# Kernel optimization log

Measured on AMD Instinct MI355X. Metric: run time of the kernel, lower is better.

## Reference

```python
import jax, jax.numpy as jnp
import numpy as np

E, H, L = 1280, 20, 8192
D = E // H


def setup_inputs() -> dict:
    key = jax.random.key(0)
    ks = jax.random.split(key, 12)
    inp = {
        "hidden_states": jax.random.normal(ks[0], (1, 1, E), jnp.float32),
        "position_ids": jax.random.randint(ks[1], (1,), 0, L, jnp.int64),
        "k_cache": jax.random.normal(ks[2], (1, H, L, D), jnp.float32),
        "v_cache": jax.random.normal(ks[3], (1, H, L, D), jnp.float32),
        "Wq": jax.random.normal(ks[4], (E, E), jnp.float32) * 0.02,
        "bq": jax.random.normal(ks[5], (E,), jnp.float32) * 0.02,
        "Wk": jax.random.normal(ks[6], (E, E), jnp.float32) * 0.02,
        "Wv": jax.random.normal(ks[7], (E, E), jnp.float32) * 0.02,
        "bv": jax.random.normal(ks[8], (E,), jnp.float32) * 0.02,
        "Wo": jax.random.normal(ks[9], (E, E), jnp.float32) * 0.02,
        "bo": jax.random.normal(ks[10], (E,), jnp.float32) * 0.02,
    }
    return inp


def reference(hidden_states, position_ids, k_cache, v_cache, Wq, bq, Wk, Wv, bv, Wo, bo):
    # hidden_states: [1,1,E]; k_cache/v_cache: [1,H,L,D]; position_ids: [1] int
    h = k_cache.shape[1]
    d = k_cache.shape[3]
    l = k_cache.shape[2]
    e = h * d
    scale = jnp.asarray(d, hidden_states.dtype) ** -0.5

    def split_heads(x):  # [1,1,E] -> [1,H,1,D]
        return x.reshape(1, 1, h, d).transpose(0, 2, 1, 3)

    q = split_heads((hidden_states @ Wq.T + bq) * scale)
    k_new = split_heads(hidden_states @ Wk.T)          # k_proj has no bias
    v_new = split_heads(hidden_states @ Wv.T + bv)

    pos = position_ids.reshape(())
    positions = jnp.arange(l)
    write_mask = (positions == pos)[None, None, :, None]   # [1,1,L,1]
    # masked broadcast-update of the KV cache (same math as cache*(1-m)+new*m)
    new_k_cache = jnp.where(write_mask, k_new, k_cache)    # [1,H,L,D]
    new_v_cache = jnp.where(write_mask, v_new, v_cache)

    scores = jnp.einsum('bhqd,bhkd->bhqk', q, new_k_cache)  # [1,H,1,L]
    causal = jnp.where(positions[None, None, None, :] <= pos,
                       jnp.asarray(0.0, scores.dtype),
                       jnp.asarray(-1e9, scores.dtype))
    attn = jax.nn.softmax(scores + causal, axis=-1)
    out = jnp.einsum('bhqk,bhkd->bhqd', attn, new_v_cache)  # [1,H,1,D]
    out = out.transpose(0, 2, 1, 3).reshape(1, 1, e)
    out = out @ Wo.T + bo
    return out, new_k_cache, new_v_cache
```

## Files before the change

kernel.cpp:

```cpp
#include <hip/hip_runtime.h>

#define E 1280
#define H 20
#define L 8192
#define D 64
#define CHUNK 256
#define NCHUNK (L / CHUNK)

__global__ void qkv_kernel(const float* __restrict__ hs,
                           const float* __restrict__ Wq, const float* __restrict__ bq,
                           const float* __restrict__ Wk,
                           const float* __restrict__ Wv, const float* __restrict__ bv,
                           float* __restrict__ qkv) {
    int row_global = blockIdx.x * 4 + (threadIdx.x >> 6);
    int lane = threadIdx.x & 63;
    int mat = row_global / E;
    int row = row_global - mat * E;
    const float* W = (mat == 0) ? Wq : (mat == 1) ? Wk : Wv;
    const float4* Wrow = (const float4*)(W + (size_t)row * E);
    const float4* h4 = (const float4*)hs;
    float sum = 0.f;
#pragma unroll
    for (int i = 0; i < 5; ++i) {
        int idx = lane + 64 * i;
        float4 w4 = Wrow[idx];
        float4 x4 = h4[idx];
        sum += w4.x * x4.x + w4.y * x4.y + w4.z * x4.z + w4.w * x4.w;
    }
#pragma unroll
    for (int off = 32; off > 0; off >>= 1) sum += __shfl_down(sum, off, 64);
    if (lane == 0) {
        float val;
        if (mat == 0)      val = (sum + bq[row]) * 0.125f;
        else if (mat == 1) val = sum;
        else               val = sum + bv[row];
        qkv[mat * E + row] = val;
    }
}

__global__ void kv_kernel(const float* __restrict__ kc, const float* __restrict__ vc,
                          const float* __restrict__ qkv, const int* __restrict__ pos_p,
                          float* __restrict__ out_k, float* __restrict__ out_v,
                          float* __restrict__ cmax, float* __restrict__ csum,
                          float* __restrict__ o_part) {
    int h = blockIdx.x / NCHUNK;
    int c = blockIdx.x - h * NCHUNK;
    int pos = pos_p[0];
    int wave = threadIdx.x >> 6;
    int lane = threadIdx.x & 63;
    int rr = lane >> 4;
    int cc = lane & 15;

    __shared__ float s_lds[CHUNK];
    __shared__ float sacc[4][D];
    __shared__ float smax[4];
    __shared__ float spsum[4];

    float4 q4  = ((const float4*)qkv)[h * 16 + cc];
    float4 kn4 = ((const float4*)(qkv + E))[h * 16 + cc];
    float4 vn4 = ((const float4*)(qkv + 2 * E))[h * 16 + cc];

    size_t base = ((size_t)h * L + (size_t)c * CHUNK) * D;
    const float* kbase = kc + base;
    const float* vbase = vc + base;
    float* okbase = out_k + base;
    float* ovbase = out_v + base;
    int l0 = c * CHUNK;

    float lmax = -INFINITY;
#pragma unroll 4
    for (int it = 0; it < CHUNK / 16; ++it) {
        int r = it * 16 + wave * 4 + rr;
        int l = l0 + r;
        float4 k4 = ((const float4*)(kbase + r * D))[cc];
        if (l == pos) k4 = kn4;
        ((float4*)(okbase + r * D))[cc] = k4;
        float p = q4.x * k4.x + q4.y * k4.y + q4.z * k4.z + q4.w * k4.w;
        p += __shfl_xor(p, 1, 16);
        p += __shfl_xor(p, 2, 16);
        p += __shfl_xor(p, 4, 16);
        p += __shfl_xor(p, 8, 16);
        float s = (l <= pos) ? p : -INFINITY;
        if (cc == 0) s_lds[r] = s;
        lmax = fmaxf(lmax, s);
    }
#pragma unroll
    for (int off = 32; off > 0; off >>= 1)
        lmax = fmaxf(lmax, __shfl_xor(lmax, off, 64));
    if (lane == 0) smax[wave] = lmax;
    __syncthreads();
    float m = fmaxf(fmaxf(smax[0], smax[1]), fmaxf(smax[2], smax[3]));

    float4 acc = {0.f, 0.f, 0.f, 0.f};
    float psum = 0.f;
#pragma unroll 4
    for (int it = 0; it < CHUNK / 16; ++it) {
        int r = it * 16 + wave * 4 + rr;
        int l = l0 + r;
        float4 v4 = ((const float4*)(vbase + r * D))[cc];
        if (l == pos) v4 = vn4;
        ((float4*)(ovbase + r * D))[cc] = v4;
        float p = (l <= pos) ? __expf(s_lds[r] - m) : 0.f;
        acc.x += p * v4.x; acc.y += p * v4.y; acc.z += p * v4.z; acc.w += p * v4.w;
        if (cc == 0) psum += p;
    }
    acc.x += __shfl_xor(acc.x, 16, 64); acc.y += __shfl_xor(acc.y, 16, 64);
    acc.z += __shfl_xor(acc.z, 16, 64); acc.w += __shfl_xor(acc.w, 16, 64);
    acc.x += __shfl_xor(acc.x, 32, 64); acc.y += __shfl_xor(acc.y, 32, 64);
    acc.z += __shfl_xor(acc.z, 32, 64); acc.w += __shfl_xor(acc.w, 32, 64);
    psum += __shfl_xor(psum, 16, 64);
    psum += __shfl_xor(psum, 32, 64);
    if (rr == 0) {
        ((float4*)&sacc[wave][cc * 4])[0] = acc;
        if (cc == 0) spsum[wave] = psum;
    }
    __syncthreads();
    if (threadIdx.x < D) {
        int d = threadIdx.x;
        float o = sacc[0][d] + sacc[1][d] + sacc[2][d] + sacc[3][d];
        o_part[((size_t)h * NCHUNK + c) * D + d] = o;
        if (d == 0) {
            cmax[h * NCHUNK + c] = m;
            csum[h * NCHUNK + c] = spsum[0] + spsum[1] + spsum[2] + spsum[3];
        }
    }
}

__global__ void combine_kernel(const float* __restrict__ cmax, const float* __restrict__ csum,
                               const float* __restrict__ o_part, float* __restrict__ attn_out) {
    int h = blockIdx.x;
    int d = threadIdx.x;
    float m = -INFINITY;
#pragma unroll
    for (int c = 0; c < NCHUNK; ++c) m = fmaxf(m, cmax[h * NCHUNK + c]);
    float denom = 0.f, o = 0.f;
#pragma unroll 4
    for (int c = 0; c < NCHUNK; ++c) {
        float mc = cmax[h * NCHUNK + c];
        float sc = (mc > -1e30f) ? __expf(mc - m) : 0.f;
        denom += csum[h * NCHUNK + c] * sc;
        o += o_part[((size_t)h * NCHUNK + c) * D + d] * sc;
    }
    attn_out[h * D + d] = o / denom;
}

__global__ void ogemv_kernel(const float* __restrict__ attn_out, const float* __restrict__ Wo,
                             const float* __restrict__ bo, float* __restrict__ out) {
    int row = blockIdx.x * 4 + (threadIdx.x >> 6);
    int lane = threadIdx.x & 63;
    const float4* Wrow = (const float4*)(Wo + (size_t)row * E);
    const float4* x4 = (const float4*)attn_out;
    float sum = 0.f;
#pragma unroll
    for (int i = 0; i < 5; ++i) {
        int idx = lane + 64 * i;
        float4 w4 = Wrow[idx];
        float4 a4 = x4[idx];
        sum += w4.x * a4.x + w4.y * a4.y + w4.z * a4.z + w4.w * a4.w;
    }
#pragma unroll
    for (int off = 32; off > 0; off >>= 1) sum += __shfl_down(sum, off, 64);
    if (lane == 0) out[row] = sum + bo[row];
}

extern "C" void kernel_launch(void* const* d_in, const int* in_sizes, int n_in,
                              void* d_out, int out_size, void* d_ws, size_t ws_size,
                              hipStream_t stream) {
    const float* hs  = (const float*)d_in[0];
    const int*   pos = (const int*)d_in[1];
    const float* kc  = (const float*)d_in[2];
    const float* vc  = (const float*)d_in[3];
    const float* Wq  = (const float*)d_in[4];
    const float* bq  = (const float*)d_in[5];
    const float* Wk  = (const float*)d_in[6];
    const float* Wv  = (const float*)d_in[7];
    const float* bv  = (const float*)d_in[8];
    const float* Wo  = (const float*)d_in[9];
    const float* bo  = (const float*)d_in[10];

    float* out   = (float*)d_out;
    float* out_k = out + E;
    float* out_v = out_k + (size_t)H * L * D;

    float* ws       = (float*)d_ws;
    float* qkv      = ws;
    float* cmax     = qkv + 3 * E;
    float* csum     = cmax + H * NCHUNK;
    float* o_part   = csum + H * NCHUNK;
    float* attn_out = o_part + (size_t)H * NCHUNK * D;

    qkv_kernel<<<3 * E / 4, 256, 0, stream>>>(hs, Wq, bq, Wk, Wv, bv, qkv);
    kv_kernel<<<H * NCHUNK, 256, 0, stream>>>(kc, vc, qkv, pos, out_k, out_v,
                                              cmax, csum, o_part);
    combine_kernel<<<H, 64, 0, stream>>>(cmax, csum, o_part, attn_out);
    ogemv_kernel<<<E / 4, 256, 0, stream>>>(attn_out, Wo, bo, out);
}
```

Measured before the change: 42.94 us.

## Halve attention chunk, use nontemporal cache-copy stores, and compute softmax weights through LDS

Chunk size drops from 256 to 128, doubling the number of blocks for the bandwidth-bound KV copy and attention pass. The per-row shuffle reductions of q·k are replaced by writing partial dot products to a padded LDS array, then one thread per row sums them and computes the exp weight once. The copies of the K and V caches into the outputs now use nontemporal stores so the streaming writes do not pollute cache. In exchange the kernel adds barriers and LDS traffic, and the combine step has twice as many partial results to merge.

```diff
diff --git a/kernel.cpp b/kernel.cpp
--- a/kernel.cpp
+++ b/kernel.cpp
@@ -4,8 +4,10 @@
 #define H 20
 #define L 8192
 #define D 64
-#define CHUNK 256
+#define CHUNK 128
 #define NCHUNK (L / CHUNK)
+
+typedef float f4 __attribute__((ext_vector_type(4)));
 
 __global__ void qkv_kernel(const float* __restrict__ hs,
                            const float* __restrict__ Wq, const float* __restrict__ bq,
@@ -46,15 +48,17 @@
     int h = blockIdx.x / NCHUNK;
     int c = blockIdx.x - h * NCHUNK;
     int pos = pos_p[0];
-    int wave = threadIdx.x >> 6;
-    int lane = threadIdx.x & 63;
-    int rr = lane >> 4;
-    int cc = lane & 15;
-
-    __shared__ float s_lds[CHUNK];
+    int tid = threadIdx.x;
+    int wave = tid >> 6;
+    int lane = tid & 63;
+    int cc = tid & 15;
+    int rg = tid >> 4;
+
+    __shared__ float s_part[CHUNK][17];
+    __shared__ float s_w[CHUNK];
+    __shared__ float smax4[4];
+    __shared__ float spsum[4];
     __shared__ float sacc[4][D];
-    __shared__ float smax[4];
-    __shared__ float spsum[4];
 
     float4 q4  = ((const float4*)qkv)[h * 16 + cc];
     float4 kn4 = ((const float4*)(qkv + E))[h * 16 + cc];
@@ -67,59 +71,66 @@
     float* ovbase = out_v + base;
     int l0 = c * CHUNK;
 
-    float lmax = -INFINITY;
-#pragma unroll 4
+#pragma unroll
     for (int it = 0; it < CHUNK / 16; ++it) {
-        int r = it * 16 + wave * 4 + rr;
+        int r = it * 16 + rg;
         int l = l0 + r;
         float4 k4 = ((const float4*)(kbase + r * D))[cc];
         if (l == pos) k4 = kn4;
-        ((float4*)(okbase + r * D))[cc] = k4;
-        float p = q4.x * k4.x + q4.y * k4.y + q4.z * k4.z + q4.w * k4.w;
-        p += __shfl_xor(p, 1, 16);
-        p += __shfl_xor(p, 2, 16);
-        p += __shfl_xor(p, 4, 16);
-        p += __shfl_xor(p, 8, 16);
-        float s = (l <= pos) ? p : -INFINITY;
-        if (cc == 0) s_lds[r] = s;
-        lmax = fmaxf(lmax, s);
-    }
+        f4 kv = {k4.x, k4.y, k4.z, k4.w};
+        __builtin_nontemporal_store(kv, (f4*)(okbase + r * D) + cc);
+        s_part[r][cc] = k4.x * q4.x + k4.y * q4.y + k4.z * q4.z + k4.w * q4.w;
+    }
+    __syncthreads();
+
+    float s = -INFINITY;
+    if (tid < CHUNK) {
+        float sum = 0.f;
+#pragma unroll
+        for (int i = 0; i < 16; ++i) sum += s_part[tid][i];
+        s = (l0 + tid <= pos) ? sum : -INFINITY;
+    }
+    float lm = s;
 #pragma unroll
     for (int off = 32; off > 0; off >>= 1)
-        lmax = fmaxf(lmax, __shfl_xor(lmax, off, 64));
-    if (lane == 0) smax[wave] = lmax;
-    __syncthreads();
-    float m = fmaxf(fmaxf(smax[0], smax[1]), fmaxf(smax[2], smax[3]));
+        lm = fmaxf(lm, __shfl_xor(lm, off, 64));
+    if (lane == 0) smax4[wave] = lm;
+    __syncthreads();
+    float m = fmaxf(fmaxf(smax4[0], smax4[1]), fmaxf(smax4[2], smax4[3]));
+
+    float p = 0.f;
+    if (tid < CHUNK) {
+        p = (s > -1e30f) ? __expf(s - m) : 0.f;
+        s_w[tid] = p;
+    }
+    float ps = p;
+#pragma unroll
+    for (int off = 32; off > 0; off >>= 1) ps += __shfl_xor(ps, off, 64);
+    if (lane == 0) spsum[wave] = ps;
+    __syncthreads();
 
     float4 acc = {0.f, 0.f, 0.f, 0.f};
-    float psum = 0.f;
-#pragma unroll 4
+#pragma unroll
     for (int it = 0; it < CHUNK / 16; ++it) {
-        int r = it * 16 + wave * 4 + rr;
+        int r = it * 16 + rg;
         int l = l0 + r;
         float4 v4 = ((const float4*)(vbase + r * D))[cc];
         if (l == pos) v4 = vn4;
-        ((float4*)(ovbase + r * D))[cc] = v4;
-        float p = (l <= pos) ? __expf(s_lds[r] - m) : 0.f;
-        acc.x += p * v4.x; acc.y += p * v4.y; acc.z += p * v4.z; acc.w += p * v4.w;
-        if (cc == 0) psum += p;
+        f4 vv = {v4.x, v4.y, v4.z, v4.w};
+        __builtin_nontemporal_store(vv, (f4*)(ovbase + r * D) + cc);
+        float w = s_w[r];
+        acc.x += w * v4.x; acc.y += w * v4.y; acc.z += w * v4.z; acc.w += w * v4.w;
     }
     acc.x += __shfl_xor(acc.x, 16, 64); acc.y += __shfl_xor(acc.y, 16, 64);
     acc.z += __shfl_xor(acc.z, 16, 64); acc.w += __shfl_xor(acc.w, 16, 64);
     acc.x += __shfl_xor(acc.x, 32, 64); acc.y += __shfl_xor(acc.y, 32, 64);
     acc.z += __shfl_xor(acc.z, 32, 64); acc.w += __shfl_xor(acc.w, 32, 64);
-    psum += __shfl_xor(psum, 16, 64);
-    psum += __shfl_xor(psum, 32, 64);
-    if (rr == 0) {
-        ((float4*)&sacc[wave][cc * 4])[0] = acc;
-        if (cc == 0) spsum[wave] = psum;
-    }
-    __syncthreads();
-    if (threadIdx.x < D) {
-        int d = threadIdx.x;
-        float o = sacc[0][d] + sacc[1][d] + sacc[2][d] + sacc[3][d];
-        o_part[((size_t)h * NCHUNK + c) * D + d] = o;
-        if (d == 0) {
+    if ((lane >> 4) == 0) ((float4*)&sacc[wave][cc * 4])[0] = acc;
+    __syncthreads();
+    if (tid < D) {
+        float o = sacc[0][tid] + sacc[1][tid] + sacc[2][tid] + sacc[3][tid];
+        o_part[((size_t)h * NCHUNK + c) * D + tid] = o;
+        if (tid == 0) {
             cmax[h * NCHUNK + c] = m;
             csum[h * NCHUNK + c] = spsum[0] + spsum[1] + spsum[2] + spsum[3];
         }
```

After: 45.13 us. +5.1%, slower.

## Make each wave own a 64-row chunk, dropping block syncs and LDS in attention

Applied to the files above, without the earlier changes.

The attention kernel now gives each wave its own 64-row split-softmax chunk. Scores stay in registers, and the wave computes its own max and sum, so the LDS score buffer and both __syncthreads go away. This produces four times more partials per head. The combine kernel is widened to 256 threads that reduce four chunk groups through shared memory. The extra combine traffic and higher register pressure from the unrolled 16-element score arrays are the tradeoff.

```diff
diff --git a/kernel.cpp b/kernel.cpp
--- a/kernel.cpp
+++ b/kernel.cpp
@@ -4,8 +4,9 @@
 #define H 20
 #define L 8192
 #define D 64
-#define CHUNK 256
-#define NCHUNK (L / CHUNK)
+#define WCHUNK 64
+#define NCH (L / WCHUNK)
+#define BLOCKS_PER_HEAD (L / 256)
 
 __global__ void qkv_kernel(const float* __restrict__ hs,
                            const float* __restrict__ Wq, const float* __restrict__ bq,
@@ -43,105 +44,112 @@
                           float* __restrict__ out_k, float* __restrict__ out_v,
                           float* __restrict__ cmax, float* __restrict__ csum,
                           float* __restrict__ o_part) {
-    int h = blockIdx.x / NCHUNK;
-    int c = blockIdx.x - h * NCHUNK;
-    int pos = pos_p[0];
+    int blk = blockIdx.x;
+    int h = blk / BLOCKS_PER_HEAD;
+    int cb = blk - h * BLOCKS_PER_HEAD;
     int wave = threadIdx.x >> 6;
     int lane = threadIdx.x & 63;
     int rr = lane >> 4;
     int cc = lane & 15;
-
-    __shared__ float s_lds[CHUNK];
-    __shared__ float sacc[4][D];
-    __shared__ float smax[4];
-    __shared__ float spsum[4];
+    int chunk = cb * 4 + wave;
+    int l0 = chunk * WCHUNK;
+    int pos = pos_p[0];
 
     float4 q4  = ((const float4*)qkv)[h * 16 + cc];
     float4 kn4 = ((const float4*)(qkv + E))[h * 16 + cc];
     float4 vn4 = ((const float4*)(qkv + 2 * E))[h * 16 + cc];
 
-    size_t base = ((size_t)h * L + (size_t)c * CHUNK) * D;
+    size_t base = ((size_t)h * L + l0) * D;
     const float* kbase = kc + base;
     const float* vbase = vc + base;
     float* okbase = out_k + base;
     float* ovbase = out_v + base;
-    int l0 = c * CHUNK;
-
-    float lmax = -INFINITY;
-#pragma unroll 4
-    for (int it = 0; it < CHUNK / 16; ++it) {
-        int r = it * 16 + wave * 4 + rr;
+
+    float sc[16];
+#pragma unroll
+    for (int it = 0; it < 16; ++it) {
+        int r = it * 4 + rr;
         int l = l0 + r;
         float4 k4 = ((const float4*)(kbase + r * D))[cc];
         if (l == pos) k4 = kn4;
         ((float4*)(okbase + r * D))[cc] = k4;
-        float p = q4.x * k4.x + q4.y * k4.y + q4.z * k4.z + q4.w * k4.w;
-        p += __shfl_xor(p, 1, 16);
-        p += __shfl_xor(p, 2, 16);
-        p += __shfl_xor(p, 4, 16);
-        p += __shfl_xor(p, 8, 16);
-        float s = (l <= pos) ? p : -INFINITY;
-        if (cc == 0) s_lds[r] = s;
-        lmax = fmaxf(lmax, s);
-    }
-#pragma unroll
-    for (int off = 32; off > 0; off >>= 1)
-        lmax = fmaxf(lmax, __shfl_xor(lmax, off, 64));
-    if (lane == 0) smax[wave] = lmax;
-    __syncthreads();
-    float m = fmaxf(fmaxf(smax[0], smax[1]), fmaxf(smax[2], smax[3]));
+        float p = k4.x * q4.x + k4.y * q4.y + k4.z * q4.z + k4.w * q4.w;
+        p += __shfl_xor(p, 1, 64);
+        p += __shfl_xor(p, 2, 64);
+        p += __shfl_xor(p, 4, 64);
+        p += __shfl_xor(p, 8, 64);
+        sc[it] = (l <= pos) ? p : -INFINITY;
+    }
+
+    float m = sc[0];
+#pragma unroll
+    for (int it = 1; it < 16; ++it) m = fmaxf(m, sc[it]);
+    m = fmaxf(m, __shfl_xor(m, 16, 64));
+    m = fmaxf(m, __shfl_xor(m, 32, 64));
+
+    float psum = 0.f;
+#pragma unroll
+    for (int it = 0; it < 16; ++it) {
+        float w = (sc[it] > -1e30f) ? __expf(sc[it] - m) : 0.f;
+        sc[it] = w;
+        psum += w;
+    }
+    psum += __shfl_xor(psum, 16, 64);
+    psum += __shfl_xor(psum, 32, 64);
 
     float4 acc = {0.f, 0.f, 0.f, 0.f};
-    float psum = 0.f;
-#pragma unroll 4
-    for (int it = 0; it < CHUNK / 16; ++it) {
-        int r = it * 16 + wave * 4 + rr;
+#pragma unroll
+    for (int it = 0; it < 16; ++it) {
+        int r = it * 4 + rr;
         int l = l0 + r;
         float4 v4 = ((const float4*)(vbase + r * D))[cc];
         if (l == pos) v4 = vn4;
         ((float4*)(ovbase + r * D))[cc] = v4;
-        float p = (l <= pos) ? __expf(s_lds[r] - m) : 0.f;
-        acc.x += p * v4.x; acc.y += p * v4.y; acc.z += p * v4.z; acc.w += p * v4.w;
-        if (cc == 0) psum += p;
+        float w = sc[it];
+        acc.x += w * v4.x; acc.y += w * v4.y; acc.z += w * v4.z; acc.w += w * v4.w;
     }
     acc.x += __shfl_xor(acc.x, 16, 64); acc.y += __shfl_xor(acc.y, 16, 64);
     acc.z += __shfl_xor(acc.z, 16, 64); acc.w += __shfl_xor(acc.w, 16, 64);
     acc.x += __shfl_xor(acc.x, 32, 64); acc.y += __shfl_xor(acc.y, 32, 64);
     acc.z += __shfl_xor(acc.z, 32, 64); acc.w += __shfl_xor(acc.w, 32, 64);
-    psum += __shfl_xor(psum, 16, 64);
-    psum += __shfl_xor(psum, 32, 64);
+
     if (rr == 0) {
-        ((float4*)&sacc[wave][cc * 4])[0] = acc;
-        if (cc == 0) spsum[wave] = psum;
-    }
-    __syncthreads();
-    if (threadIdx.x < D) {
-        int d = threadIdx.x;
-        float o = sacc[0][d] + sacc[1][d] + sacc[2][d] + sacc[3][d];
-        o_part[((size_t)h * NCHUNK + c) * D + d] = o;
-        if (d == 0) {
-            cmax[h * NCHUNK + c] = m;
-            csum[h * NCHUNK + c] = spsum[0] + spsum[1] + spsum[2] + spsum[3];
-        }
+        float* op = o_part + ((size_t)h * NCH + chunk) * WCHUNK;
+        ((float4*)op)[cc] = acc;
+    }
+    if (lane == 0) {
+        cmax[h * NCH + chunk] = m;
+        csum[h * NCH + chunk] = psum;
     }
 }
 
 __global__ void combine_kernel(const float* __restrict__ cmax, const float* __restrict__ csum,
                                const float* __restrict__ o_part, float* __restrict__ attn_out) {
     int h = blockIdx.x;
-    int d = threadIdx.x;
+    int tid = threadIdx.x;
+    int d = tid & 63;
+    int cg = tid >> 6;
+    __shared__ float so[4][D];
+    __shared__ float sden[4];
+
     float m = -INFINITY;
-#pragma unroll
-    for (int c = 0; c < NCHUNK; ++c) m = fmaxf(m, cmax[h * NCHUNK + c]);
+#pragma unroll 8
+    for (int c = 0; c < NCH; ++c) m = fmaxf(m, cmax[h * NCH + c]);
+
     float denom = 0.f, o = 0.f;
 #pragma unroll 4
-    for (int c = 0; c < NCHUNK; ++c) {
-        float mc = cmax[h * NCHUNK + c];
-        float sc = (mc > -1e30f) ? __expf(mc - m) : 0.f;
-        denom += csum[h * NCHUNK + c] * sc;
-        o += o_part[((size_t)h * NCHUNK + c) * D + d] * sc;
-    }
-    attn_out[h * D + d] = o / denom;
+    for (int c = cg * 32; c < cg * 32 + 32; ++c) {
+        float mc = cmax[h * NCH + c];
+        float sf = (mc > -1e30f) ? __expf(mc - m) : 0.f;
+        denom += csum[h * NCH + c] * sf;
+        o += o_part[((size_t)h * NCH + c) * WCHUNK + d] * sf;
+    }
+    so[cg][d] = o;
+    if (d == 0) sden[cg] = denom;
+    __syncthreads();
+    if (cg == 0)
+        attn_out[h * D + d] = (so[0][d] + so[1][d] + so[2][d] + so[3][d]) /
+                              (sden[0] + sden[1] + sden[2] + sden[3]);
 }
 
 __global__ void ogemv_kernel(const float* __restrict__ attn_out, const float* __restrict__ Wo,
@@ -185,13 +193,13 @@
     float* ws       = (float*)d_ws;
     float* qkv      = ws;
     float* cmax     = qkv + 3 * E;
-    float* csum     = cmax + H * NCHUNK;
-    float* o_part   = csum + H * NCHUNK;
-    float* attn_out = o_part + (size_t)H * NCHUNK * D;
+    float* csum     = cmax + H * NCH;
+    float* o_part   = csum + H * NCH;
+    float* attn_out = o_part + (size_t)H * NCH * WCHUNK;
 
     qkv_kernel<<<3 * E / 4, 256, 0, stream>>>(hs, Wq, bq, Wk, Wv, bv, qkv);
-    kv_kernel<<<H * NCHUNK, 256, 0, stream>>>(kc, vc, qkv, pos, out_k, out_v,
-                                              cmax, csum, o_part);
-    combine_kernel<<<H, 64, 0, stream>>>(cmax, csum, o_part, attn_out);
+    kv_kernel<<<H * BLOCKS_PER_HEAD, 256, 0, stream>>>(kc, vc, qkv, pos, out_k, out_v,
+                                                       cmax, csum, o_part);
+    combine_kernel<<<H, 256, 0, stream>>>(cmax, csum, o_part, attn_out);
     ogemv_kernel<<<E / 4, 256, 0, stream>>>(attn_out, Wo, bo, out);
 }
```

New measurement: 53.83 us. 25.4% more time.
